# Performance work log

Hardware: AMD Instinct MI355X
Metric: run time of the kernel (lower is better)

Reference implementation:

```python
import jax, jax.numpy as jnp
import numpy as np

P = 16        # patch size
IMG = 224     # image H=W
C = 3         # channels
D = 768       # projection_dim (= patch flatten dim here)
H = 12        # num heads
M = D // 4    # new_size = flattened_size / shrink_ratio(4) = 192
L = 6         # transformer layers
N = (IMG // P) ** 2   # 196 patches
FF = 3072     # dense_units[0]
HEAD = 512    # dense_units[2]
NCLS = 1000
EPS = 1e-6
B = 32


def setup_inputs() -> dict:
    key = jax.random.key(0)
    ks = iter(jax.random.split(key, 40))
    u = lambda shape, s=0.02: jax.random.uniform(next(ks), shape, jnp.float32, -s, s)
    image = jax.random.normal(next(ks), (B, IMG, IMG, C), jnp.float32)
    return dict(
        image=image,
        patch_w=u((P * P * C, D)), patch_b=u((D,)), pos_emb=u((N, D)),
        qw=u((L, D, M, H)), qb=jnp.zeros((L, M, H), jnp.float32),
        kw=u((L, D, M, H)), kb=jnp.zeros((L, M, H), jnp.float32),
        vw=u((L, D, M, H)), vb=jnp.zeros((L, M, H), jnp.float32),
        ow1=u((L, H * N, N)), ob1=jnp.zeros((L, M, N), jnp.float32),
        ow2=u((L, M, D)), ob2=jnp.zeros((L, N, D), jnp.float32),
        d1w=u((L, D, FF)), d1b=u((L, FF)),
        d2w=u((L, FF, D)), d2b=u((L, D)),
        head_w=u((N * D, HEAD), 0.005), head_b=u((HEAD,)),
        cls_w=u((HEAD, NCLS)), cls_b=u((NCLS,)),
    )


def _ln(x):
    # ViT_Custom_LayerNormalization: moments over axes [0,1,2] (all elements of [B,N,D])
    m = jnp.mean(x)
    v = jnp.mean(jnp.square(x - m))
    return (x - m) / jnp.sqrt(v + EPS)


def _gelu(x):
    return jax.nn.gelu(x, approximate=False)  # keras 'gelu' default is exact


def _forward(image, patch_w, patch_b, pos_emb, qw, qb, kw, kb, vw, vb,
             ow1, ob1, ow2, ob2, d1w, d1b, d2w, d2b, head_w, head_b, cls_w, cls_b):
    b = image.shape[0]
    # tf.image.extract_patches with VALID, stride=patch: [B,N,p*p*C] row-major patches
    patches = image.reshape(b, IMG // P, P, IMG // P, P, C)
    patches = patches.transpose(0, 1, 3, 2, 4, 5).reshape(b, N, P * P * C)
    x = patches @ patch_w + patch_b + pos_emb  # patch encode + pos embedding
    scale = 1.0 / np.float32(np.sqrt(D))       # key_dim = projection_dim
    for l in range(L):
        x1 = _ln(x)
        # per-head 3-D tensordot projections: [B,N,D] x [D,M,H] -> [B,N,M,H]
        q = jnp.einsum('bnd,dmh->bnmh', x1, qw[l]) + qb[l]
        k = jnp.einsum('bnd,dmh->bnmh', x1, kw[l]) + kb[l]
        v = jnp.einsum('bnd,dmh->bnmh', x1, vw[l]) + vb[l]
        att = jnp.einsum('bnmh,bNmh->bhnN', q, k) * scale  # [B,H,N,N]
        a = jax.nn.softmax(att, axis=-1)
        # attn @ V, then the module's transpose/unstack-concat -> [B,M,H*N] head-major
        o = jnp.einsum('bhnN,bNmh->bmhn', a, v).reshape(b, M, H * N)
        t = (o @ ow1[l] + ob1[l]).transpose(0, 2, 1)  # [B,N,M]
        attn_out = t @ ow2[l] + ob2[l]                # [B,N,D]
        x2 = attn_out + x
        x3 = _ln(x2)
        h = _gelu(x3 @ d1w[l] + d1b[l])
        h = _gelu(h @ d2w[l] + d2b[l])
        x = h + x2
    x = _ln(x)
    flat = x.reshape(b, N * D)
    feat = _gelu(flat @ head_w + head_b)
    return feat @ cls_w + cls_b  # [B, NCLS]


def reference(image, patch_w, patch_b, pos_emb, qw, qb, kw, kb, vw, vb,
              ow1, ob1, ow2, ob2, d1w, d1b, d2w, d2b, head_w, head_b, cls_w, cls_b):
    return _forward(image, patch_w, patch_b, pos_emb, qw, qb, kw, kb, vw, vb,
                    ow1, ob1, ow2, ob2, d1w, d1b, d2w, d2b, head_w, head_b, cls_w, cls_b)
```

## Files before the change

kernel.cpp:

```cpp
#include <hip/hip_runtime.h>
#include <cmath>

#define BZ    32
#define NP    196
#define DDIM  768
#define NHEAD 12
#define MDIM  192
#define NLAY  6
#define FFDIM 3072
#define HEADU 512
#define NCLS  1000
#define KHEAD 150528
#define BND   4816896

typedef __bf16 bf16_t;
typedef __bf16 bf16x8 __attribute__((ext_vector_type(8)));
typedef __bf16 bf16x4 __attribute__((ext_vector_type(4)));
typedef float  f32x4  __attribute__((ext_vector_type(4)));
typedef float  f32x2  __attribute__((ext_vector_type(2)));

#define OB_X      0L
#define OB_R      19267584L
#define OB_XB     38535168L
#define OB_XQKV   48168960L
#define OB_VT     134873088L
#define OB_O      165543936L
#define OB_TT     194641920L
#define OB_T      197050368L
#define OB_WQKV   199458816L
#define OB_WO1    210075648L
#define OB_WO2    211288064L
#define OB_WD1    211582976L
#define OB_WD2    216301568L
#define OB_WPAT   221020160L
#define OB_BQKV   222199808L
#define OB_RED    222227456L
#define OB_STAT   222235648L
#define OB_FEAT   222235904L

#define VT_SSTRIDE  39936L
#define ATTN_LDSP   93184
#define ATTN_LDS    143360
#define XROW        13824

__device__ __forceinline__ float gelu_exact(float x){
    return 0.5f * x * (1.0f + erff(x * 0.70710678118654752f));
}

__device__ __forceinline__ void gld16(const void* g, void* l){
    __builtin_amdgcn_global_load_lds((const __attribute__((address_space(1))) void*)g,
                                     (__attribute__((address_space(3))) void*)l, 16, 0, 0);
}

__global__ void __launch_bounds__(256)
patch_extract_k(const float* __restrict__ img, bf16_t* __restrict__ out)
{
    long idx = (long)blockIdx.x * 256 + threadIdx.x;
    if (idx >= (long)BND) return;
    int k = (int)(idx % DDIM);
    long bn = idx / DDIM;
    int n = (int)(bn % NP);
    int b = (int)(bn / NP);
    int c  = k % 3;
    int pj = (k / 3) % 16;
    int pi = k / 48;
    int gi = n / 14, gj = n % 14;
    long src = (((long)(b * 224 + gi * 16 + pi)) * 224 + (gj * 16 + pj)) * 3 + c;
    out[idx] = (bf16_t)img[src];
}

__global__ void __launch_bounds__(256)
wconv_k(const float* __restrict__ in, bf16_t* __restrict__ out,
        int IR, int IC, long OLD, int perm, int padTo)
{
    __shared__ float tile[32][33];
    int tid = threadIdx.x, tx = tid & 31, ty = tid >> 5;
    int c0 = blockIdx.x * 32, r0 = blockIdx.y * 32;
    #pragma unroll
    for (int i = 0; i < 4; i++){
        int r = r0 + ty + 8*i, c = c0 + tx;
        tile[ty + 8*i][tx] = (r < IR && c < IC) ? in[(long)r * IC + c] : 0.f;
    }
    __syncthreads();
    #pragma unroll
    for (int i = 0; i < 4; i++){
        int c = c0 + ty + 8*i, r = r0 + tx;
        if (c < IC && r < padTo){
            long pc = perm ? (long)(c % 12) * 192 + c / 12 : (long)c;
            out[pc * OLD + r] = (bf16_t)tile[tx][ty + 8*i];
        }
    }
}

__global__ void __launch_bounds__(256)
gather_bias_k(const float* __restrict__ qb, const float* __restrict__ kb,
              const float* __restrict__ vb, float* __restrict__ out)
{
    int tid = blockIdx.x * 256 + threadIdx.x;
    if (tid >= 6912) return;
    int g = tid / 2304, w = tid % 2304;
    int h = w / 192, m = w % 192;
    const float* src = (g == 0) ? qb : (g == 1) ? kb : vb;
    out[tid] = src[m * 12 + h];
}

__global__ void __launch_bounds__(256)
zero_pad_o_k(bf16_t* __restrict__ o)
{
    int idx = blockIdx.x * 256 + threadIdx.x;
    if (idx >= 6144*16) return;
    int r = idx >> 4, j = idx & 15;
    o[(long)r * 2368 + 2352 + j] = (bf16_t)0.f;
}

__global__ void __launch_bounds__(256)
tr_v_k(const bf16_t* __restrict__ X, bf16_t* __restrict__ VT)
{
    __shared__ bf16_t tile[32][33];
    int tid = threadIdx.x, tx = tid & 31, ty = tid >> 5;
    int s = blockIdx.z, b = s & 31, h = s >> 5;
    int m0 = blockIdx.x * 32, n0 = blockIdx.y * 32;
    #pragma unroll
    for (int i = 0; i < 4; i++){
        int r = n0 + ty + 8*i, c = m0 + tx;
        tile[ty + 8*i][tx] = (r < 196) ?
            X[(long)(b*196 + r) * 6912 + 4608 + h*192 + c] : (bf16_t)0.f;
    }
    __syncthreads();
    #pragma unroll
    for (int i = 0; i < 4; i++){
        int m = m0 + ty + 8*i, n = n0 + tx;
        if (n < 208)
            VT[(long)s * VT_SSTRIDE + (long)m * 208 + n] = tile[tx][ty + 8*i];
    }
}

__global__ void __launch_bounds__(256)
tr_t_k(const bf16_t* __restrict__ TT, bf16_t* __restrict__ Tt)
{
    __shared__ bf16_t tile[32][33];
    int tid = threadIdx.x, tx = tid & 31, ty = tid >> 5;
    int b = blockIdx.z;
    int m0 = blockIdx.x * 32, n0 = blockIdx.y * 32;
    #pragma unroll
    for (int i = 0; i < 4; i++){
        int r = m0 + ty + 8*i, c = n0 + tx;
        tile[ty + 8*i][tx] = (c < 196) ? TT[(long)b*37632 + (long)r*196 + c] : (bf16_t)0.f;
    }
    __syncthreads();
    #pragma unroll
    for (int i = 0; i < 4; i++){
        int n = n0 + ty + 8*i, m = m0 + tx;
        if (n < 196)
            Tt[((long)b*196 + n)*192 + m] = tile[tx][ty + 8*i];
    }
}

__global__ void __launch_bounds__(256)
reduce_k(const float* __restrict__ x, float* __restrict__ psum, float* __restrict__ psq)
{
    __shared__ float ss[256], sq[256];
    float s = 0.f, q = 0.f;
    const long n4 = BND / 4;
    const float4* x4 = (const float4*)x;
    for (long i = (long)blockIdx.x * 256 + threadIdx.x; i < n4; i += (long)gridDim.x * 256){
        float4 v = x4[i];
        s += v.x + v.y + v.z + v.w;
        q += v.x*v.x + v.y*v.y + v.z*v.z + v.w*v.w;
    }
    ss[threadIdx.x] = s; sq[threadIdx.x] = q;
    __syncthreads();
    for (int st = 128; st > 0; st >>= 1){
        if (threadIdx.x < st){ ss[threadIdx.x] += ss[threadIdx.x+st]; sq[threadIdx.x] += sq[threadIdx.x+st]; }
        __syncthreads();
    }
    if (threadIdx.x == 0){ psum[blockIdx.x] = ss[0]; psq[blockIdx.x] = sq[0]; }
}

__global__ void __launch_bounds__(256)
stats_k(const float* __restrict__ psum, const float* __restrict__ psq, float* __restrict__ stats)
{
    __shared__ float ss[256], sq[256];
    float s = 0.f, q = 0.f;
    for (int i = threadIdx.x; i < 1024; i += 256){ s += psum[i]; q += psq[i]; }
    ss[threadIdx.x] = s; sq[threadIdx.x] = q;
    __syncthreads();
    for (int st = 128; st > 0; st >>= 1){
        if (threadIdx.x < st){ ss[threadIdx.x] += ss[threadIdx.x+st]; sq[threadIdx.x] += sq[threadIdx.x+st]; }
        __syncthreads();
    }
    if (threadIdx.x == 0){
        float mean = ss[0] / (float)BND;
        float var  = sq[0] / (float)BND - mean * mean;
        stats[0] = mean;
        stats[1] = rsqrtf(var + 1e-6f);
    }
}

__global__ void __launch_bounds__(256)
ln_apply_k(const float* __restrict__ x, bf16_t* __restrict__ yb, float* __restrict__ yf,
           const float* __restrict__ stats)
{
    long i = (long)blockIdx.x * 256 + threadIdx.x;
    if (i >= BND / 4) return;
    float mean = stats[0], inv = stats[1];
    float4 v = ((const float4*)x)[i];
    v.x = (v.x - mean) * inv;
    v.y = (v.y - mean) * inv;
    v.z = (v.z - mean) * inv;
    v.w = (v.w - mean) * inv;
    bf16x4 o4 = { (bf16_t)v.x, (bf16_t)v.y, (bf16_t)v.z, (bf16_t)v.w };
    ((bf16x4*)yb)[i] = o4;
    if (yf) ((float4*)yf)[i] = v;
}

__global__ void __launch_bounds__(256)
attn_fused_k(const bf16_t* __restrict__ XQKV, const bf16_t* __restrict__ VT,
             bf16_t* __restrict__ O)
{
    extern __shared__ char lds[];
    const int tid = threadIdx.x, lane = tid & 63, w = tid >> 6;
    const int fr = lane & 15, kc = lane >> 4;
    const int s = blockIdx.y, qhalf = blockIdx.x;
    const int q0 = qhalf * 112;
    const int b = s & 31, h = s >> 5;
    const float scale = 0.03608439182435161f;
    const char* Xb = (const char*)XQKV + (long)(b*196) * XROW;
    const char* Qs = Xb + h*384;
    const char* Ks = Xb + 4608 + h*384;
    const char* Vs = (const char*)(VT + (long)s * VT_SSTRIDE);

    for (int t = 0; t < 23; t++){
        int idx = t*256 + tid;
        if (idx < 5824){
            int row = idx / 28, sl = idx - row*28;
            bool val = (sl < 24) && (row < 196);
            const char* src = Ks + (val ? ((long)row*XROW + ((sl*16) ^ ((row & 7) << 4))) : 0);
            gld16(src, lds + idx*16);
        }
    }
    asm volatile("s_waitcnt vmcnt(0)");
    __syncthreads();

    float pv_all[2][13][4];
    #pragma unroll
    for (int ii = 0; ii < 2; ii++){
        int i = w + ii*4;
        if (i >= 7) continue;
        f32x4 sa[13];
        #pragma unroll
        for (int f = 0; f < 13; f++) sa[f] = (f32x4){0.f,0.f,0.f,0.f};
        int qr = q0 + i*16 + fr; if (qr > 195) qr = 195;
        #pragma unroll
        for (int c = 0; c < 6; c++){
            bf16x8 av = *(const bf16x8*)(Qs + (long)qr*XROW + c*64 + kc*16);
            #pragma unroll
            for (int f = 0; f < 13; f++){
                int krow = f*16 + fr;
                bf16x8 bv = *(const bf16x8*)(lds + krow*448 + ((c*64 + kc*16) ^ ((krow & 7) << 4)));
                sa[f] = __builtin_amdgcn_mfma_f32_16x16x32_bf16(av, bv, sa[f], 0, 0, 0);
            }
        }
        #pragma unroll
        for (int r = 0; r < 4; r++){
            float mx = -1e30f;
            #pragma unroll
            for (int f = 0; f < 13; f++)
                if (f*16 + fr < 196) mx = fmaxf(mx, sa[f][r] * scale);
            mx = fmaxf(mx, __shfl_xor(mx, 1));
            mx = fmaxf(mx, __shfl_xor(mx, 2));
            mx = fmaxf(mx, __shfl_xor(mx, 4));
            mx = fmaxf(mx, __shfl_xor(mx, 8));
            float sum = 0.f;
            #pragma unroll
            for (int f = 0; f < 13; f++){
                float pv = (f*16 + fr < 196) ? __expf(sa[f][r] * scale - mx) : 0.f;
                pv_all[ii][f][r] = pv; sum += pv;
            }
            sum += __shfl_xor(sum, 1);
            sum += __shfl_xor(sum, 2);
            sum += __shfl_xor(sum, 4);
            sum += __shfl_xor(sum, 8);
            float inv = 1.f / sum;
            #pragma unroll
            for (int f = 0; f < 13; f++) pv_all[ii][f][r] *= inv;
        }
        #pragma unroll
        for (int f = 0; f < 13; f++)
            #pragma unroll
            for (int r = 0; r < 4; r++){
                int row = i*16 + kc*4 + r;
                int cb = (f*16 + fr) * 2;
                int a = ATTN_LDSP + row*448 + (cb < 384 ? (cb ^ ((row & 7) << 4)) : cb);
                *(bf16_t*)(lds + a) = (bf16_t)pv_all[ii][f][r];
            }
        if (lane < 32){
            int row = i*16 + (lane >> 1);
            *(f32x4*)(lds + ATTN_LDSP + row*448 + 416 + (lane & 1)*16) = (f32x4){0.f,0.f,0.f,0.f};
        }
    }
    __syncthreads();

    for (int t = 0; t < 21; t++){
        int idx = t*256 + tid;
        int row = idx / 28, sl = idx - row*28;
        bool val = (sl < 26);
        int cb = (sl < 24) ? ((sl*16) ^ ((row & 7) << 4)) : sl*16;
        const char* src = Vs + (val ? (row*416 + cb) : 0);
        gld16(src, lds + idx*16);
    }
    asm volatile("s_waitcnt vmcnt(0)");
    __syncthreads();

    f32x4 oa2[2][12];
    #pragma unroll
    for (int ii = 0; ii < 2; ii++){
        int i = w + ii*4;
        #pragma unroll
        for (int f = 0; f < 12; f++) oa2[ii][f] = (f32x4){0.f,0.f,0.f,0.f};
        if (i >= 7) continue;
        #pragma unroll
        for (int c = 0; c < 7; c++){
            int prow = i*16 + fr;
            int cb = c*64 + kc*16;
            int acb = (cb < 384) ? (cb ^ ((prow & 7) << 4)) : cb;
            bf16x8 av = *(const bf16x8*)(lds + ATTN_LDSP + prow*448 + acb);
            #pragma unroll
            for (int f = 0; f < 12; f++){
                int vrow = f*16 + fr;
                int bcb = (cb < 384) ? (cb ^ ((vrow & 7) << 4)) : cb;
                bf16x8 bv = *(const bf16x8*)(lds + vrow*448 + bcb);
                oa2[ii][f] = __builtin_amdgcn_mfma_f32_16x16x32_bf16(av, bv, oa2[ii][f], 0, 0, 0);
            }
        }
    }
    __syncthreads();

    #pragma unroll
    for (int ii = 0; ii < 2; ii++){
        int i = w + ii*4;
        if (i >= 7) continue;
        #pragma unroll
        for (int f = 0; f < 12; f++){
            int m = f*16 + fr;
            #pragma unroll
            for (int r = 0; r < 4; r++){
                int nl = i*16 + kc*4 + r;
                *(bf16_t*)(lds + m*232 + nl*2) = (bf16_t)oa2[ii][f][r];
            }
        }
    }
    __syncthreads();
    const int nch = (qhalf == 0) ? 28 : 21;
    const int total = 192 * nch;
    char* ob = (char*)O + ((long)(b*192))*4736 + ((long)(h*196 + q0))*2;
    for (int idx = tid; idx < total; idx += 256){
        int m = idx / nch, ch = idx - m*nch;
        f32x2 v2 = *(const f32x2*)(lds + m*232 + ch*8);
        *(f32x2*)(ob + (long)m*4736 + ch*8) = v2;
    }
}

__global__ void __launch_bounds__(256)
mfma_gemm_k(const bf16_t* __restrict__ A, long ldA, long sA,
            const bf16_t* __restrict__ B, long ldB, long sB,
            void* __restrict__ C, long ldC, long sC,
            const float* __restrict__ Cadd,
            const float* __restrict__ bias1,
            const float* __restrict__ bias2, int b2mod, int b2ld,
            int Md, int Nd, int Kd, float alpha, int doGelu, int mode)
{
    __shared__ bf16_t sm[2][2][128][32];
    const int tid = threadIdx.x;
    const int lane = tid & 63, w = tid >> 6;
    const int wm = w >> 1, wn = w & 1;
    const int z = blockIdx.z;

    int n2d = gridDim.x * gridDim.y;
    int flat = blockIdx.x + gridDim.x * blockIdx.y;
    int q8 = n2d >> 3, r8 = n2d & 7;
    int xcd = flat & 7, pos = flat >> 3;
    int id2 = (xcd < r8 ? xcd*(q8+1) : r8*(q8+1) + (xcd-r8)*q8) + pos;
    int bx = id2 % gridDim.x, by = id2 / gridDim.x;

    const int row0 = by * 128, col0 = bx * 128;

    const bf16_t* Ab = A + (long)z * sA + (long)row0 * ldA;
    const bf16_t* Bb = B + (long)z * sB + (long)col0 * ldB;

    f32x4 acc[4][4];
    #pragma unroll
    for (int i = 0; i < 4; i++)
        #pragma unroll
        for (int j = 0; j < 4; j++)
            acc[i][j] = (f32x4){0.f, 0.f, 0.f, 0.f};

    const int fr = lane & 15, kc = lane >> 4;
    const int swz = (fr >> 1) & 3;
    int aOff[4], bOff[4];
    #pragma unroll
    for (int i = 0; i < 4; i++){
        aOff[i] = (wm*64 + i*16 + fr) * 64 + ((kc ^ swz) << 4);
        bOff[i] = (wn*64 + i*16 + fr) * 64 + ((kc ^ swz) << 4);
    }

    auto stage = [&](int buf, int kt){
        long kOff = (long)kt * 32;
        #pragma unroll
        for (int r = 0; r < 2; r++){
            int idx = r*256 + tid;
            int row = idx >> 2, cp = idx & 3;
            int cc = cp ^ ((row >> 1) & 3);
            gld16((const void*)(Ab + (long)row*ldA + kOff + cc*8), (void*)&sm[buf][0][row][cp*8]);
            gld16((const void*)(Bb + (long)row*ldB + kOff + cc*8), (void*)&sm[buf][1][row][cp*8]);
        }
    };

    const int nt = Kd >> 5;
    stage(0, 0);
    __syncthreads();
    int cur = 0;
    for (int t = 0; t < nt; t++){
        if (t + 1 < nt) stage(cur ^ 1, t + 1);
        const char* baseA = (const char*)sm + cur * 16384;
        const char* baseB = baseA + 8192;
        bf16x8 av[4], bv[4];
        #pragma unroll
        for (int i = 0; i < 4; i++){
            av[i] = *(const bf16x8*)(baseA + aOff[i]);
            bv[i] = *(const bf16x8*)(baseB + bOff[i]);
        }
        #pragma unroll
        for (int i = 0; i < 4; i++)
            #pragma unroll
            for (int j = 0; j < 4; j++)
                acc[i][j] = __builtin_amdgcn_mfma_f32_16x16x32_bf16(av[i], bv[j], acc[i][j], 0, 0, 0);
        __syncthreads();
        cur ^= 1;
    }

    #pragma unroll
    for (int i = 0; i < 4; i++){
        int gmb = row0 + wm*64 + i*16 + kc*4;
        #pragma unroll
        for (int j = 0; j < 4; j++){
            int gn = col0 + wn*64 + j*16 + fr;
            if (gn >= Nd) continue;
            #pragma unroll
            for (int r = 0; r < 4; r++){
                int gm = gmb + r;
                if (gm >= Md) continue;
                float v = alpha * acc[i][j][r];
                if (bias1) v += bias1[gn];
                if (bias2) v += bias2[(long)(gm % b2mod) * b2ld + gn];
                if (doGelu) v = gelu_exact(v);
                if (mode == 0){
                    long off = (long)z*sC + (long)gm*ldC + gn;
                    if (Cadd) v += Cadd[off];
                    ((float*)C)[off] = v;
                } else {
                    ((bf16_t*)C)[(long)z*sC + (long)gm*ldC + gn] = (bf16_t)v;
                }
            }
        }
    }
}

__global__ void __launch_bounds__(256)
head_splitk_k(const float* __restrict__ A, const float* __restrict__ W, float* __restrict__ feat)
{
    __shared__ float As[16][36];
    __shared__ float Bs[16][68];
    int col0 = blockIdx.x * 64;
    long kbase = (long)blockIdx.y * 2352;
    int tid = threadIdx.x, tx = tid & 15, ty = tid >> 4;
    float acc[2][4] = {};
    for (int k0 = 0; k0 < 2352; k0 += 16){
        #pragma unroll
        for (int u = 0; u < 2; u++){
            int idx = tid * 2 + u;
            int m = idx >> 4, kk = idx & 15;
            As[kk][m] = A[(long)m * KHEAD + kbase + k0 + kk];
        }
        #pragma unroll
        for (int u = 0; u < 4; u++){
            int idx = tid * 4 + u;
            int kk = idx >> 6, n = idx & 63;
            Bs[kk][n] = W[(kbase + k0 + kk) * 512 + col0 + n];
        }
        __syncthreads();
        #pragma unroll
        for (int kk = 0; kk < 16; kk++){
            float a0 = As[kk][ty*2], a1 = As[kk][ty*2+1];
            float b0 = Bs[kk][tx*4], b1 = Bs[kk][tx*4+1], b2 = Bs[kk][tx*4+2], b3 = Bs[kk][tx*4+3];
            acc[0][0] += a0*b0; acc[0][1] += a0*b1; acc[0][2] += a0*b2; acc[0][3] += a0*b3;
            acc[1][0] += a1*b0; acc[1][1] += a1*b1; acc[1][2] += a1*b2; acc[1][3] += a1*b3;
        }
        __syncthreads();
    }
    #pragma unroll
    for (int i = 0; i < 2; i++)
        #pragma unroll
        for (int j = 0; j < 4; j++)
            atomicAdd(&feat[(ty*2 + i) * 512 + col0 + tx*4 + j], acc[i][j]);
}

__global__ void __launch_bounds__(256)
head_finish_k(float* __restrict__ feat, const float* __restrict__ hb)
{
    int i = blockIdx.x * 256 + threadIdx.x;
    if (i < BZ * HEADU) feat[i] = gelu_exact(feat[i] + hb[i & 511]);
}

__global__ void __launch_bounds__(256)
cls_k(const float* __restrict__ feat, const float* __restrict__ W,
      const float* __restrict__ bias, float* __restrict__ out)
{
    __shared__ float fs[512];
    int b = blockIdx.y;
    int j = blockIdx.x * 256 + threadIdx.x;
    for (int i = threadIdx.x; i < 512; i += 256) fs[i] = feat[b * 512 + i];
    __syncthreads();
    if (j < NCLS){
        float s = bias[j];
        for (int k = 0; k < 512; k++) s += fs[k] * W[(long)k * NCLS + j];
        out[b * NCLS + j] = s;
    }
}

extern "C" void kernel_launch(void* const* d_in, const int* in_sizes, int n_in,
                              void* d_out, int out_size, void* d_ws, size_t ws_size,
                              hipStream_t stream)
{
    const float* image   = (const float*)d_in[0];
    const float* patch_w = (const float*)d_in[1];
    const float* patch_b = (const float*)d_in[2];
    const float* pos_emb = (const float*)d_in[3];
    const float* qw  = (const float*)d_in[4];
    const float* qb  = (const float*)d_in[5];
    const float* kw  = (const float*)d_in[6];
    const float* kb  = (const float*)d_in[7];
    const float* vw  = (const float*)d_in[8];
    const float* vb  = (const float*)d_in[9];
    const float* ow1 = (const float*)d_in[10];
    const float* ob1 = (const float*)d_in[11];
    const float* ow2 = (const float*)d_in[12];
    const float* ob2 = (const float*)d_in[13];
    const float* d1w = (const float*)d_in[14];
    const float* d1b = (const float*)d_in[15];
    const float* d2w = (const float*)d_in[16];
    const float* d2b = (const float*)d_in[17];
    const float* head_w = (const float*)d_in[18];
    const float* head_b = (const float*)d_in[19];
    const float* cls_w  = (const float*)d_in[20];
    const float* cls_b  = (const float*)d_in[21];

    char* wsb = (char*)d_ws;
    float*  X    = (float*) (wsb + OB_X);
    float*  R    = (float*) (wsb + OB_R);
    bf16_t* XB   = (bf16_t*)(wsb + OB_XB);
    bf16_t* XQKV = (bf16_t*)(wsb + OB_XQKV);
    bf16_t* VT   = (bf16_t*)(wsb + OB_VT);
    bf16_t* O    = (bf16_t*)(wsb + OB_O);
    bf16_t* TT   = (bf16_t*)(wsb + OB_TT);
    bf16_t* Tt   = (bf16_t*)(wsb + OB_T);
    bf16_t* H1   = XQKV;
    bf16_t* PATB = XQKV;
    bf16_t* WQKV = (bf16_t*)(wsb + OB_WQKV);
    bf16_t* WO1  = (bf16_t*)(wsb + OB_WO1);
    bf16_t* WO2  = (bf16_t*)(wsb + OB_WO2);
    bf16_t* WD1  = (bf16_t*)(wsb + OB_WD1);
    bf16_t* WD2  = (bf16_t*)(wsb + OB_WD2);
    bf16_t* WPAT = (bf16_t*)(wsb + OB_WPAT);
    float*  BQKV = (float*) (wsb + OB_BQKV);
    float*  RSUM = (float*) (wsb + OB_RED);
    float*  RSQ  = RSUM + 1024;
    float*  STAT = (float*) (wsb + OB_STAT);
    float*  FEAT = (float*) (wsb + OB_FEAT);
    float*  out  = (float*)d_out;

    hipFuncSetAttribute((const void*)attn_fused_k,
                        hipFuncAttributeMaxDynamicSharedMemorySize, ATTN_LDS);

    auto mg = [&](const bf16_t* A, long ldA, long sA, const bf16_t* B, long ldB, long sB,
                  void* C, long ldC, long sC, const float* Cadd, const float* b1,
                  const float* b2, int b2mod, int b2ld,
                  int Md, int Nd, int Kd, int nb, float alpha, int gelu, int mode){
        dim3 g((Nd + 127) / 128, (Md + 127) / 128, nb);
        mfma_gemm_k<<<g, 256, 0, stream>>>(A, ldA, sA, B, ldB, sB, C, ldC, sC,
                                           Cadd, b1, b2, b2mod, b2ld,
                                           Md, Nd, Kd, alpha, gelu, mode);
    };
    auto wconv = [&](const float* in, bf16_t* o_, int IR, int IC, int perm, long OLD, int padTo){
        dim3 g((IC + 31) / 32, (padTo + 31) / 32);
        wconv_k<<<g, 256, 0, stream>>>(in, o_, IR, IC, OLD, perm, padTo);
    };
    auto layernorm = [&](const float* in, bf16_t* ob, float* of){
        reduce_k<<<1024, 256, 0, stream>>>(in, RSUM, RSQ);
        stats_k<<<1, 256, 0, stream>>>(RSUM, RSQ, STAT);
        ln_apply_k<<<4704, 256, 0, stream>>>(in, ob, of, STAT);
    };

    wconv(patch_w, WPAT, 768, 768, 0, 768, 768);
    patch_extract_k<<<18816, 256, 0, stream>>>(image, PATB);
    mg(PATB, 768, 0, WPAT, 768, 0, X, 768, 0,
       nullptr, patch_b, pos_emb, 196, 768, 6272, 768, 768, 1, 1.f, 0, 0);
    zero_pad_o_k<<<384, 256, 0, stream>>>(O);

    for (int l = 0; l < NLAY; l++){
        wconv(qw + (long)l*768*2304, WQKV, 768, 2304, 1, 768, 768);
        wconv(kw + (long)l*768*2304, WQKV + 2304L*768, 768, 2304, 1, 768, 768);
        wconv(vw + (long)l*768*2304, WQKV + 4608L*768, 768, 2304, 1, 768, 768);
        gather_bias_k<<<27, 256, 0, stream>>>(qb + l*2304, kb + l*2304, vb + l*2304, BQKV);
        wconv(ow1 + (long)l*2352*196, WO1, 2352, 196, 0, 2368, 2368);
        wconv(ow2 + (long)l*192*768, WO2, 192, 768, 0, 192, 192);
        wconv(d1w + (long)l*768*3072, WD1, 768, 3072, 0, 768, 768);
        wconv(d2w + (long)l*3072*768, WD2, 3072, 768, 0, 3072, 3072);

        layernorm(X, XB, nullptr);
        mg(XB, 768, 0, WQKV, 768, 0, XQKV, 6912, 0, nullptr, BQKV, nullptr, 1, 1,
           6272, 6912, 768, 1, 1.f, 0, 1);
        tr_v_k<<<dim3(6, 7, 384), 256, 0, stream>>>(XQKV, VT);
        attn_fused_k<<<dim3(2, 384), 256, ATTN_LDS, stream>>>(XQKV, VT, O);
        mg(O, 2368, 192L*2368, WO1, 2368, 0, TT, 196, 37632, nullptr, nullptr,
           ob1 + (long)l*192*196, 192, 196, 192, 196, 2368, 32, 1.f, 0, 1);
        tr_t_k<<<dim3(6, 7, 32), 256, 0, stream>>>(TT, Tt);
        mg(Tt, 192, 0, WO2, 192, 0, R, 768, 0, X, nullptr,
           ob2 + (long)l*196*768, 196, 768, 6272, 768, 192, 1, 1.f, 0, 0);
        layernorm(R, XB, nullptr);
        mg(XB, 768, 0, WD1, 768, 0, H1, 3072, 0, nullptr, d1b + l*3072, nullptr, 1, 1,
           6272, 3072, 768, 1, 1.f, 1, 1);
        mg(H1, 3072, 0, WD2, 3072, 0, X, 768, 0, R, d2b + l*768, nullptr, 1, 1,
           6272, 768, 3072, 1, 1.f, 1, 0);
    }

    layernorm(X, XB, R);
    hipMemsetAsync(FEAT, 0, BZ * HEADU * sizeof(float), stream);
    head_splitk_k<<<dim3(8, 64), 256, 0, stream>>>(R, head_w, FEAT);
    head_finish_k<<<64, 256, 0, stream>>>(FEAT, head_b);
    cls_k<<<dim3(4, 32), 256, 0, stream>>>(FEAT, cls_w, cls_b, out);
    (void)in_sizes; (void)n_in; (void)out_size; (void)ws_size;
}
```

Before: 3.671 ms.

## Batch weight conversions, fuse LN stats, drop transpose, triple-buffer GEMM K-loop

All six layers' weights are converted to bf16 in a few batched launches up front instead of eight launches per layer. The ob1 bias is pre-transposed so the ow1 GEMM can write the [N,M] layout directly, which removes the tr_t_k transpose and its intermediate buffer. The stats kernel is folded into ln_apply, with every block redoing the 1024-partial reduction. The MFMA GEMM moves from double to triple buffered LDS with explicit vmcnt waits, raw barriers and setprio, so loads run two tiles ahead. The cost is more workspace, more LDS per block, and a redundant reduction in each LN-apply block.

```diff
diff --git a/kernel.cpp b/kernel.cpp
--- a/kernel.cpp
+++ b/kernel.cpp
@@ -25,18 +25,17 @@
 #define OB_XQKV   48168960L
 #define OB_VT     134873088L
 #define OB_O      165543936L
-#define OB_TT     194641920L
-#define OB_T      197050368L
-#define OB_WQKV   199458816L
-#define OB_WO1    210075648L
-#define OB_WO2    211288064L
-#define OB_WD1    211582976L
-#define OB_WD2    216301568L
-#define OB_WPAT   221020160L
-#define OB_BQKV   222199808L
-#define OB_RED    222227456L
-#define OB_STAT   222235648L
-#define OB_FEAT   222235904L
+#define OB_T      194641920L
+#define OB_WQKV   197050368L
+#define OB_WO1    260751360L
+#define OB_WO2    268025856L
+#define OB_WD1    269795328L
+#define OB_WD2    298106880L
+#define OB_WPAT   326418432L
+#define OB_BQKV   327598080L
+#define OB_OB1T   327763968L
+#define OB_RED    328667136L
+#define OB_FEAT   328675584L
 
 #define VT_SSTRIDE  39936L
 #define ATTN_LDSP   93184
@@ -71,15 +70,17 @@
 
 __global__ void __launch_bounds__(256)
 wconv_k(const float* __restrict__ in, bf16_t* __restrict__ out,
-        int IR, int IC, long OLD, int perm, int padTo)
+        int IR, int IC, long OLD, int perm, int padTo, long inZ, long outZ)
 {
     __shared__ float tile[32][33];
     int tid = threadIdx.x, tx = tid & 31, ty = tid >> 5;
     int c0 = blockIdx.x * 32, r0 = blockIdx.y * 32;
+    const float* inz = in + (long)blockIdx.z * inZ;
+    bf16_t* outz = out + (long)blockIdx.z * outZ;
     #pragma unroll
     for (int i = 0; i < 4; i++){
         int r = r0 + ty + 8*i, c = c0 + tx;
-        tile[ty + 8*i][tx] = (r < IR && c < IC) ? in[(long)r * IC + c] : 0.f;
+        tile[ty + 8*i][tx] = (r < IR && c < IC) ? inz[(long)r * IC + c] : 0.f;
     }
     __syncthreads();
     #pragma unroll
@@ -87,7 +88,7 @@
         int c = c0 + ty + 8*i, r = r0 + tx;
         if (c < IC && r < padTo){
             long pc = perm ? (long)(c % 12) * 192 + c / 12 : (long)c;
-            out[pc * OLD + r] = (bf16_t)tile[tx][ty + 8*i];
+            outz[pc * OLD + r] = (bf16_t)tile[tx][ty + 8*i];
         }
     }
 }
@@ -97,11 +98,22 @@
               const float* __restrict__ vb, float* __restrict__ out)
 {
     int tid = blockIdx.x * 256 + threadIdx.x;
+    int l = blockIdx.y;
     if (tid >= 6912) return;
     int g = tid / 2304, w = tid % 2304;
     int h = w / 192, m = w % 192;
     const float* src = (g == 0) ? qb : (g == 1) ? kb : vb;
-    out[tid] = src[m * 12 + h];
+    out[l*6912 + tid] = src[l*2304 + m * 12 + h];
+}
+
+__global__ void __launch_bounds__(256)
+tr_bias_k(const float* __restrict__ ob1, float* __restrict__ out)
+{
+    int idx = blockIdx.x * 256 + threadIdx.x;
+    int l = blockIdx.y;
+    if (idx >= 37632) return;
+    int n = idx / 192, m = idx - n*192;
+    out[(long)l*37632 + idx] = ob1[(long)l*37632 + m*196 + n];
 }
 
 __global__ void __launch_bounds__(256)
@@ -132,27 +144,6 @@
         int m = m0 + ty + 8*i, n = n0 + tx;
         if (n < 208)
             VT[(long)s * VT_SSTRIDE + (long)m * 208 + n] = tile[tx][ty + 8*i];
-    }
-}
-
-__global__ void __launch_bounds__(256)
-tr_t_k(const bf16_t* __restrict__ TT, bf16_t* __restrict__ Tt)
-{
-    __shared__ bf16_t tile[32][33];
-    int tid = threadIdx.x, tx = tid & 31, ty = tid >> 5;
-    int b = blockIdx.z;
-    int m0 = blockIdx.x * 32, n0 = blockIdx.y * 32;
-    #pragma unroll
-    for (int i = 0; i < 4; i++){
-        int r = m0 + ty + 8*i, c = n0 + tx;
-        tile[ty + 8*i][tx] = (c < 196) ? TT[(long)b*37632 + (long)r*196 + c] : (bf16_t)0.f;
-    }
-    __syncthreads();
-    #pragma unroll
-    for (int i = 0; i < 4; i++){
-        int n = n0 + ty + 8*i, m = m0 + tx;
-        if (n < 196)
-            Tt[((long)b*196 + n)*192 + m] = tile[tx][ty + 8*i];
     }
 }
 
@@ -178,32 +169,24 @@
 }
 
 __global__ void __launch_bounds__(256)
-stats_k(const float* __restrict__ psum, const float* __restrict__ psq, float* __restrict__ stats)
-{
-    __shared__ float ss[256], sq[256];
+ln_apply_k(const float* __restrict__ x, bf16_t* __restrict__ yb, float* __restrict__ yf,
+           const float* __restrict__ psum, const float* __restrict__ psq)
+{
+    __shared__ float sred[8];
+    int tid = threadIdx.x;
     float s = 0.f, q = 0.f;
-    for (int i = threadIdx.x; i < 1024; i += 256){ s += psum[i]; q += psq[i]; }
-    ss[threadIdx.x] = s; sq[threadIdx.x] = q;
-    __syncthreads();
-    for (int st = 128; st > 0; st >>= 1){
-        if (threadIdx.x < st){ ss[threadIdx.x] += ss[threadIdx.x+st]; sq[threadIdx.x] += sq[threadIdx.x+st]; }
-        __syncthreads();
-    }
-    if (threadIdx.x == 0){
-        float mean = ss[0] / (float)BND;
-        float var  = sq[0] / (float)BND - mean * mean;
-        stats[0] = mean;
-        stats[1] = rsqrtf(var + 1e-6f);
-    }
-}
-
-__global__ void __launch_bounds__(256)
-ln_apply_k(const float* __restrict__ x, bf16_t* __restrict__ yb, float* __restrict__ yf,
-           const float* __restrict__ stats)
-{
-    long i = (long)blockIdx.x * 256 + threadIdx.x;
+    for (int i = tid; i < 1024; i += 256){ s += psum[i]; q += psq[i]; }
+    #pragma unroll
+    for (int off = 32; off > 0; off >>= 1){ s += __shfl_xor(s, off); q += __shfl_xor(q, off); }
+    if ((tid & 63) == 0){ sred[(tid>>6)*2] = s; sred[(tid>>6)*2+1] = q; }
+    __syncthreads();
+    s = sred[0] + sred[2] + sred[4] + sred[6];
+    q = sred[1] + sred[3] + sred[5] + sred[7];
+    float mean = s / (float)BND;
+    float inv  = rsqrtf(q / (float)BND - mean*mean + 1e-6f);
+
+    long i = (long)blockIdx.x * 256 + tid;
     if (i >= BND / 4) return;
-    float mean = stats[0], inv = stats[1];
     float4 v = ((const float4*)x)[i];
     v.x = (v.x - mean) * inv;
     v.y = (v.y - mean) * inv;
@@ -370,7 +353,7 @@
             const float* __restrict__ bias2, int b2mod, int b2ld,
             int Md, int Nd, int Kd, float alpha, int doGelu, int mode)
 {
-    __shared__ bf16_t sm[2][2][128][32];
+    __shared__ bf16_t sm[3][2][128][32];
     const int tid = threadIdx.x;
     const int lane = tid & 63, w = tid >> 6;
     const int wm = w >> 1, wn = w & 1;
@@ -418,10 +401,14 @@
 
     const int nt = Kd >> 5;
     stage(0, 0);
-    __syncthreads();
-    int cur = 0;
+    stage(1, 1);
+    asm volatile("s_waitcnt vmcnt(4)" ::: "memory");
+    __builtin_amdgcn_s_barrier();
+    __builtin_amdgcn_sched_barrier(0);
+
     for (int t = 0; t < nt; t++){
-        if (t + 1 < nt) stage(cur ^ 1, t + 1);
+        int cur = t % 3;
+        if (t + 2 < nt) stage((t + 2) % 3, t + 2);
         const char* baseA = (const char*)sm + cur * 16384;
         const char* baseB = baseA + 8192;
         bf16x8 av[4], bv[4];
@@ -430,13 +417,17 @@
             av[i] = *(const bf16x8*)(baseA + aOff[i]);
             bv[i] = *(const bf16x8*)(baseB + bOff[i]);
         }
+        __builtin_amdgcn_s_setprio(1);
         #pragma unroll
         for (int i = 0; i < 4; i++)
             #pragma unroll
             for (int j = 0; j < 4; j++)
                 acc[i][j] = __builtin_amdgcn_mfma_f32_16x16x32_bf16(av[i], bv[j], acc[i][j], 0, 0, 0);
-        __syncthreads();
-        cur ^= 1;
+        __builtin_amdgcn_s_setprio(0);
+        if (t + 2 < nt)      asm volatile("s_waitcnt vmcnt(4)" ::: "memory");
+        else if (t + 1 < nt) asm volatile("s_waitcnt vmcnt(0)" ::: "memory");
+        __builtin_amdgcn_s_barrier();
+        __builtin_amdgcn_sched_barrier(0);
     }
 
     #pragma unroll
@@ -562,7 +553,6 @@
     bf16_t* XQKV = (bf16_t*)(wsb + OB_XQKV);
     bf16_t* VT   = (bf16_t*)(wsb + OB_VT);
     bf16_t* O    = (bf16_t*)(wsb + OB_O);
-    bf16_t* TT   = (bf16_t*)(wsb + OB_TT);
     bf16_t* Tt   = (bf16_t*)(wsb + OB_T);
     bf16_t* H1   = XQKV;
     bf16_t* PATB = XQKV;
@@ -573,9 +563,9 @@
     bf16_t* WD2  = (bf16_t*)(wsb + OB_WD2);
     bf16_t* WPAT = (bf16_t*)(wsb + OB_WPAT);
     float*  BQKV = (float*) (wsb + OB_BQKV);
+    float*  OB1T = (float*) (wsb + OB_OB1T);
     float*  RSUM = (float*) (wsb + OB_RED);
     float*  RSQ  = RSUM + 1024;
-    float*  STAT = (float*) (wsb + OB_STAT);
     float*  FEAT = (float*) (wsb + OB_FEAT);
     float*  out  = (float*)d_out;
 
@@ -591,47 +581,48 @@
                                            Cadd, b1, b2, b2mod, b2ld,
                                            Md, Nd, Kd, alpha, gelu, mode);
     };
-    auto wconv = [&](const float* in, bf16_t* o_, int IR, int IC, int perm, long OLD, int padTo){
-        dim3 g((IC + 31) / 32, (padTo + 31) / 32);
-        wconv_k<<<g, 256, 0, stream>>>(in, o_, IR, IC, OLD, perm, padTo);
+    auto wconv = [&](const float* in, bf16_t* o_, int IR, int IC, int perm, long OLD,
+                     int padTo, int nz, long inZ, long outZ){
+        dim3 g((IC + 31) / 32, (padTo + 31) / 32, nz);
+        wconv_k<<<g, 256, 0, stream>>>(in, o_, IR, IC, OLD, perm, padTo, inZ, outZ);
     };
     auto layernorm = [&](const float* in, bf16_t* ob, float* of){
         reduce_k<<<1024, 256, 0, stream>>>(in, RSUM, RSQ);
-        stats_k<<<1, 256, 0, stream>>>(RSUM, RSQ, STAT);
-        ln_apply_k<<<4704, 256, 0, stream>>>(in, ob, of, STAT);
+        ln_apply_k<<<4704, 256, 0, stream>>>(in, ob, of, RSUM, RSQ);
     };
 
-    wconv(patch_w, WPAT, 768, 768, 0, 768, 768);
+    wconv(patch_w, WPAT, 768, 768, 0, 768, 768, 1, 0, 0);
+    wconv(qw, WQKV,               768, 2304, 1, 768, 768, 6, 768L*2304, 6912L*768);
+    wconv(kw, WQKV + 2304L*768,   768, 2304, 1, 768, 768, 6, 768L*2304, 6912L*768);
+    wconv(vw, WQKV + 4608L*768,   768, 2304, 1, 768, 768, 6, 768L*2304, 6912L*768);
+    wconv(ow1, WO1, 2352, 196, 0, 2368, 2368, 6, 2352L*196, 606208L);
+    wconv(ow2, WO2, 192, 768, 0, 192, 192, 6, 147456L, 147456L);
+    wconv(d1w, WD1, 768, 3072, 0, 768, 768, 6, 2359296L, 2359296L);
+    wconv(d2w, WD2, 3072, 768, 0, 3072, 3072, 6, 2359296L, 2359296L);
+    gather_bias_k<<<dim3(27, 6), 256, 0, stream>>>(qb, kb, vb, BQKV);
+    tr_bias_k<<<dim3(147, 6), 256, 0, stream>>>(ob1, OB1T);
+
     patch_extract_k<<<18816, 256, 0, stream>>>(image, PATB);
     mg(PATB, 768, 0, WPAT, 768, 0, X, 768, 0,
        nullptr, patch_b, pos_emb, 196, 768, 6272, 768, 768, 1, 1.f, 0, 0);
     zero_pad_o_k<<<384, 256, 0, stream>>>(O);
 
     for (int l = 0; l < NLAY; l++){
-        wconv(qw + (long)l*768*2304, WQKV, 768, 2304, 1, 768, 768);
-        wconv(kw + (long)l*768*2304, WQKV + 2304L*768, 768, 2304, 1, 768, 768);
-        wconv(vw + (long)l*768*2304, WQKV + 4608L*768, 768, 2304, 1, 768, 768);
-        gather_bias_k<<<27, 256, 0, stream>>>(qb + l*2304, kb + l*2304, vb + l*2304, BQKV);
-        wconv(ow1 + (long)l*2352*196, WO1, 2352, 196, 0, 2368, 2368);
-        wconv(ow2 + (long)l*192*768, WO2, 192, 768, 0, 192, 192);
-        wconv(d1w + (long)l*768*3072, WD1, 768, 3072, 0, 768, 768);
-        wconv(d2w + (long)l*3072*768, WD2, 3072, 768, 0, 3072, 3072);
-
         layernorm(X, XB, nullptr);
-        mg(XB, 768, 0, WQKV, 768, 0, XQKV, 6912, 0, nullptr, BQKV, nullptr, 1, 1,
-           6272, 6912, 768, 1, 1.f, 0, 1);
+        mg(XB, 768, 0, WQKV + (long)l*6912*768, 768, 0, XQKV, 6912, 0, nullptr,
+           BQKV + l*6912, nullptr, 1, 1, 6272, 6912, 768, 1, 1.f, 0, 1);
         tr_v_k<<<dim3(6, 7, 384), 256, 0, stream>>>(XQKV, VT);
         attn_fused_k<<<dim3(2, 384), 256, ATTN_LDS, stream>>>(XQKV, VT, O);
-        mg(O, 2368, 192L*2368, WO1, 2368, 0, TT, 196, 37632, nullptr, nullptr,
-           ob1 + (long)l*192*196, 192, 196, 192, 196, 2368, 32, 1.f, 0, 1);
-        tr_t_k<<<dim3(6, 7, 32), 256, 0, stream>>>(TT, Tt);
-        mg(Tt, 192, 0, WO2, 192, 0, R, 768, 0, X, nullptr,
+        mg(WO1 + (long)l*606208, 2368, 0, O, 2368, 192L*2368, Tt, 192, 37632,
+           nullptr, nullptr, OB1T + (long)l*37632, 196, 192,
+           196, 192, 2368, 32, 1.f, 0, 1);
+        mg(Tt, 192, 0, WO2 + (long)l*147456, 192, 0, R, 768, 0, X, nullptr,
            ob2 + (long)l*196*768, 196, 768, 6272, 768, 192, 1, 1.f, 0, 0);
         layernorm(R, XB, nullptr);
-        mg(XB, 768, 0, WD1, 768, 0, H1, 3072, 0, nullptr, d1b + l*3072, nullptr, 1, 1,
-           6272, 3072, 768, 1, 1.f, 1, 1);
-        mg(H1, 3072, 0, WD2, 3072, 0, X, 768, 0, R, d2b + l*768, nullptr, 1, 1,
-           6272, 768, 3072, 1, 1.f, 1, 0);
+        mg(XB, 768, 0, WD1 + (long)l*2359296, 768, 0, H1, 3072, 0, nullptr,
+           d1b + l*3072, nullptr, 1, 1, 6272, 3072, 768, 1, 1.f, 1, 1);
+        mg(H1, 3072, 0, WD2 + (long)l*2359296, 3072, 0, X, 768, 0, R,
+           d2b + l*768, nullptr, 1, 1, 6272, 768, 3072, 1, 1.f, 1, 0);
     }
 
     layernorm(X, XB, R);
```

Result: faster. 3.426 ms (-6.7%).
